# Kernel optimization log

Hardware: AMD Instinct MI355X
Metric: run time of the kernel (lower is better)

Reference implementation:

```python
import jax, jax.numpy as jnp
import numpy as np

N = 100000      # nodes
E = 1600000     # edges (avg degree 16)
G = 500         # graphs in batch
C_IN = 128
H = 128
C_OUT = 200
N_CLASSES = 4


def _lin(k, fi, fo):
    s = 1.0 / np.sqrt(fi)
    return jax.random.uniform(k, (fi, fo), jnp.float32, -s, s)


def setup_inputs() -> dict:
    key = jax.random.key(0)
    ks = jax.random.split(key, 8)
    x = jax.random.normal(ks[0], (N, C_IN), jnp.float32)
    edge_index = jax.random.randint(ks[1], (2, E), 0, N, dtype=jnp.int64)
    edge_attr = jax.random.uniform(ks[2], (E,), jnp.float32)
    batch = jnp.sort(jax.random.randint(ks[3], (N,), 0, G, dtype=jnp.int64))
    W0 = _lin(ks[4], C_IN, H)
    W1 = _lin(ks[5], H, H)
    W2 = _lin(ks[6], H, C_OUT)
    Wp = _lin(ks[7], C_OUT, N_CLASSES)
    return dict(
        x=x, edge_index=edge_index, edge_attr=edge_attr, batch=batch,
        W0=W0, b0=jnp.zeros((H,), jnp.float32),
        W1=W1, b1=jnp.zeros((H,), jnp.float32),
        W2=W2, b2=jnp.zeros((C_OUT,), jnp.float32),
        Wp=Wp, bp=jnp.zeros((N_CLASSES,), jnp.float32),
    )


def reference(x, edge_index, edge_attr, batch, W0, b0, W1, b1, W2, b2, Wp, bp):
    n = x.shape[0]
    loop = jnp.arange(n)
    # GCNConv: add self-loops (weight 1), symmetric normalization D^-1/2 A D^-1/2
    src = jnp.concatenate([edge_index[0], loop])
    dst = jnp.concatenate([edge_index[1], loop])
    w = jnp.concatenate([edge_attr, jnp.ones((n,), x.dtype)])
    deg = jax.ops.segment_sum(w, dst, num_segments=n)
    dis = jnp.where(deg > 0, jax.lax.rsqrt(jnp.maximum(deg, 1e-12)), 0.0)
    norm = dis[src] * w * dis[dst]  # [E+N]

    def conv(h, W, b):
        h = h @ W                               # transform first (PyG GCNConv)
        msg = h[src] * norm[:, None]            # gather + scale
        return jax.ops.segment_sum(msg, dst, num_segments=n) + b

    h = jax.nn.relu(conv(x, W0, b0))
    h = jax.nn.relu(conv(h, W1, b1))
    h = conv(h, W2, b2)                         # last layer: no activation

    # global_mean_pool over graph ids
    gsum = jax.ops.segment_sum(h, batch, num_segments=G)
    cnt = jax.ops.segment_sum(jnp.ones((n,), h.dtype), batch, num_segments=G)
    pooled = gsum / jnp.maximum(cnt, 1.0)[:, None]

    return pooled @ Wp + bp  # [G, 4]
```

## Files before the change

### kernel.cpp

```cpp
#include <hip/hip_runtime.h>
#include <hip/hip_bf16.h>
#include <hip/hip_fp16.h>


#define FEAT 128
#define BSH 8
#define BCAP 8192

typedef union { int2 i2; long long u; struct { int s; float w; } e; } EdgePair;
typedef union { unsigned u; __half2 h2; } H2U;
typedef _Float16 f16x8 __attribute__((ext_vector_type(8)));
typedef float f32x4 __attribute__((ext_vector_type(4)));
typedef float f32x2 __attribute__((ext_vector_type(2)));

__device__ __forceinline__ unsigned pack2h(float a, float b) {
    return (unsigned)__half_as_ushort(__float2half_rn(a)) |
           ((unsigned)__half_as_ushort(__float2half_rn(b)) << 16);
}

__device__ __forceinline__ unsigned char to_fp8(float v) {
    int pk = __builtin_amdgcn_cvt_pk_fp8_f32(v, v, 0, false);
    return (unsigned char)(pk & 0xFF);
}

__global__ __launch_bounds__(256) void bin1_kernel(const int* __restrict__ src,
                                                   const int* __restrict__ dst,
                                                   const float* __restrict__ w,
                                                   int* __restrict__ gcnt,
                                                   int2* __restrict__ bins,
                                                   int E_, int NB) {
    __shared__ int lh[392], lofs[392], lbase[392], lcur[392];
    __shared__ unsigned sU[4096];
    __shared__ float    sW[4096];
    __shared__ unsigned short sB[4096];
    const int CHUNK = 4096;
    int base = blockIdx.x * CHUNK;
    int tid = threadIdx.x;
    for (int t = tid; t < NB; t += 256) { lh[t] = 0; lcur[t] = 0; }
    __syncthreads();
    int ds[16];
#pragma unroll
    for (int j = 0; j < 16; ++j) {
        int e = base + j * 256 + tid;
        ds[j] = (e < E_) ? dst[e] : -1;
        if (ds[j] >= 0) atomicAdd(&lh[ds[j] >> BSH], 1);
    }
    __syncthreads();
    for (int t = tid; t < NB; t += 256) {
        int run = 0;
        for (int i = 0; i < t; ++i) run += lh[i];
        lofs[t] = run;
    }
    __syncthreads();
    for (int t = tid; t < NB; t += 256)
        if (lh[t] > 0) lbase[t] = atomicAdd(&gcnt[t], lh[t]);
    __syncthreads();
#pragma unroll
    for (int j = 0; j < 16; ++j) {
        int e = base + j * 256 + tid;
        if (ds[j] >= 0) {
            int b = ds[j] >> BSH;
            int r = atomicAdd(&lcur[b], 1);
            int s = lofs[b] + r;
            sU[s] = (unsigned)src[e] | ((unsigned)(ds[j] & 255) << 20);
            sW[s] = w[e];
            sB[s] = (unsigned short)b;
        }
    }
    __syncthreads();
    int total = min(CHUNK, E_ - base);
    for (int s = tid; s < total; s += 256) {
        int b = sB[s];
        int g = lbase[b] + (s - lofs[b]);
        if (g < BCAP) {
            int2 val; val.x = (int)sU[s]; val.y = __float_as_int(sW[s]);
            bins[(size_t)b * BCAP + g] = val;
        }
    }
}

__global__ __launch_bounds__(256) void buildcsr_kernel(const int2* __restrict__ bins,
                                                       const int* __restrict__ gcnt,
                                                       int* __restrict__ rp,
                                                       float* __restrict__ dis,
                                                       unsigned* __restrict__ cv, int n) {
    __shared__ int lh[256];
    __shared__ float wsum[256];
    __shared__ int sc[256];
    __shared__ int lcur[256];
    __shared__ int red[256];
    __shared__ unsigned scv[BCAP + 256];
    int b = blockIdx.x;
    int tid = threadIdx.x;
    int node0 = b << BSH;
    int node = node0 + tid;
    bool valid = node < n;
    lh[tid] = 0;
    wsum[tid] = 1.0f;
    int part = 0;
    for (int i = tid; i < b; i += 256)
        part += min(gcnt[i], BCAP) + min(256, n - (i << BSH));
    red[tid] = part;
    __syncthreads();
    for (int off = 128; off > 0; off >>= 1) {
        if (tid < off) red[tid] += red[tid + off];
        __syncthreads();
    }
    int base = red[0];
    int m = min(gcnt[b], BCAP);
    int nvalid = min(256, n - node0);
    if (b == (int)gridDim.x - 1 && tid == 0)
        rp[n] = base + m + nvalid;
    const int2* bp = bins + (size_t)b * BCAP;
    for (int i = tid; i < m; i += 256) {
        int2 raw = bp[i];
        unsigned pk = (unsigned)raw.x;
        int dlo = pk >> 20;
        atomicAdd(&lh[dlo], 1);
        atomicAdd(&wsum[dlo], __int_as_float(raw.y));
    }
    __syncthreads();
    int cnt_t = valid ? (lh[tid] + 1) : 0;
    sc[tid] = cnt_t;
    __syncthreads();
    for (int off = 1; off < 256; off <<= 1) {
        int x = (tid >= off) ? sc[tid - off] : 0;
        __syncthreads();
        sc[tid] += x;
        __syncthreads();
    }
    int excl = sc[tid] - cnt_t;
    if (valid) {
        rp[node] = base + excl;
        dis[node] = rsqrtf(fmaxf(wsum[tid], 1e-12f));
    }
    lcur[tid] = excl;
    __syncthreads();
    for (int i = tid; i < m; i += 256) {
        int2 raw = bp[i];
        unsigned pk = (unsigned)raw.x;
        int dlo = pk >> 20;
        int pos = atomicAdd(&lcur[dlo], 1);
        unsigned hw = (unsigned)__half_as_ushort(__float2half_rn(__int_as_float(raw.y)));
        scv[pos] = (hw << 17) | (pk & 0x1FFFF);
    }
    __syncthreads();
    if (valid) {
        int pos = atomicAdd(&lcur[tid], 1);
        scv[pos] = (0x3C00u << 17) | (unsigned)node;
    }
    __syncthreads();
    int total = m + nvalid;
    for (int s = tid; s < total; s += 256)
        cv[base + s] = scv[s];
}

__global__ __launch_bounds__(256) void prep_kernel(const float* __restrict__ W0,
                                                   const float* __restrict__ W1,
                                                   const float* __restrict__ W2,
                                                   const float* __restrict__ Wp,
                                                   const float* __restrict__ b2,
                                                   const float* __restrict__ bp,
                                                   const int* __restrict__ batch,
                                                   _Float16* __restrict__ Wt0,
                                                   _Float16* __restrict__ Wt1,
                                                   float* __restrict__ Wc,
                                                   float* __restrict__ bc,
                                                   int* __restrict__ gstart,
                                                   int* __restrict__ gcnt,
                                                   int n, int G_, int NB) {
    int blk = blockIdx.x;
    if (blk < 64) {
        int tid = blk * 256 + threadIdx.x;
        int nn = tid >> 7, k = tid & 127;
        Wt0[nn * 128 + k] = (_Float16)W0[k * 128 + nn];
    } else if (blk < 128) {
        int tid = (blk - 64) * 256 + threadIdx.x;
        int nn = tid >> 7, k = tid & 127;
        Wt1[nn * 128 + k] = (_Float16)W1[k * 128 + nn];
    } else if (blk == 128) {
        for (int tid = threadIdx.x; tid < 512; tid += 256) {
            int c = tid >> 2, k = tid & 3;
            float s = 0.f;
            for (int j = 0; j < 200; ++j) s = fmaf(W2[c * 200 + j], Wp[j * 4 + k], s);
            Wc[tid] = s;
        }
        if (threadIdx.x < 4) {
            float s = bp[threadIdx.x];
            for (int j = 0; j < 200; ++j) s = fmaf(b2[j], Wp[j * 4 + threadIdx.x], s);
            bc[threadIdx.x] = s;
        }
        for (int i = threadIdx.x; i < NB; i += 256) gcnt[i] = 0;
    } else {
        int i = (blk - 129) * 256 + threadIdx.x;
        if (i >= n) return;
        int b = batch[i];
        int prev = (i == 0) ? -1 : batch[i - 1];
        for (int g = prev + 1; g <= b; ++g) gstart[g] = i;
        if (i == n - 1) {
            for (int g = b + 1; g <= G_; ++g) gstart[g] = n;
        }
    }
}

__global__ __launch_bounds__(256, 4) void gemm1_mfma(const float* __restrict__ A,
                                                     const _Float16* __restrict__ Wt,
                                                     const float* __restrict__ rowscale,
                                                     unsigned char* __restrict__ C, int M) {
    int wid = threadIdx.x >> 6, lane = threadIdx.x & 63;
    int quad = lane >> 4, l16 = lane & 15;
    int row0 = blockIdx.x * 64 + wid * 16;
    int arow = row0 + l16; if (arow >= M) arow = M - 1;
    const float* abase = A + (size_t)arow * 128 + quad * 8;
    float4 a0[4], a1[4];
#pragma unroll
    for (int kc = 0; kc < 4; ++kc) {
        a0[kc] = *(const float4*)(abase + kc * 32);
        a1[kc] = *(const float4*)(abase + kc * 32 + 4);
    }
    f16x8 af[4];
#pragma unroll
    for (int kc = 0; kc < 4; ++kc)
        af[kc] = (f16x8){ (_Float16)a0[kc].x, (_Float16)a0[kc].y, (_Float16)a0[kc].z, (_Float16)a0[kc].w,
                          (_Float16)a1[kc].x, (_Float16)a1[kc].y, (_Float16)a1[kc].z, (_Float16)a1[kc].w };
    f32x4 acc[8];
#pragma unroll
    for (int t = 0; t < 8; ++t) acc[t] = (f32x4){0.f, 0.f, 0.f, 0.f};
    const _Float16* wbase = Wt + (size_t)l16 * 128 + quad * 8;
#pragma unroll
    for (int t = 0; t < 8; ++t) {
        f16x8 bf[4];
#pragma unroll
        for (int kc = 0; kc < 4; ++kc)
            bf[kc] = *(const f16x8*)(wbase + (size_t)t * 16 * 128 + kc * 32);
#pragma unroll
        for (int kc = 0; kc < 4; ++kc)
            acc[t] = __builtin_amdgcn_mfma_f32_16x16x32_f16(af[kc], bf[kc], acc[t], 0, 0, 0);
    }
    int orow0 = row0 + quad * 4;
#pragma unroll
    for (int r = 0; r < 4; ++r) {
        int orow = orow0 + r;
        if (orow < M) {
            float sc = rowscale[orow];
#pragma unroll
            for (int t = 0; t < 8; ++t)
                C[(size_t)orow * 128 + t * 16 + l16] = to_fp8(acc[t][r] * sc);
        }
    }
}

__global__ __launch_bounds__(256, 4) void gemm2_mfma(const unsigned short* __restrict__ A,
                                                     const _Float16* __restrict__ Wt,
                                                     const float* __restrict__ rowscale,
                                                     unsigned char* __restrict__ C, int M) {
    int wid = threadIdx.x >> 6, lane = threadIdx.x & 63;
    int quad = lane >> 4, l16 = lane & 15;
    int row0 = blockIdx.x * 64 + wid * 16;
    int arow = row0 + l16; if (arow >= M) arow = M - 1;
    const _Float16* abase = (const _Float16*)A + (size_t)arow * 128 + quad * 8;
    f16x8 af[4];
#pragma unroll
    for (int kc = 0; kc < 4; ++kc)
        af[kc] = *(const f16x8*)(abase + kc * 32);
    f32x4 acc[8];
#pragma unroll
    for (int t = 0; t < 8; ++t) acc[t] = (f32x4){0.f, 0.f, 0.f, 0.f};
    const _Float16* wbase = Wt + (size_t)l16 * 128 + quad * 8;
#pragma unroll
    for (int t = 0; t < 8; ++t) {
        f16x8 bf[4];
#pragma unroll
        for (int kc = 0; kc < 4; ++kc)
            bf[kc] = *(const f16x8*)(wbase + (size_t)t * 16 * 128 + kc * 32);
#pragma unroll
        for (int kc = 0; kc < 4; ++kc)
            acc[t] = __builtin_amdgcn_mfma_f32_16x16x32_f16(af[kc], bf[kc], acc[t], 0, 0, 0);
    }
    int orow0 = row0 + quad * 4;
#pragma unroll
    for (int r = 0; r < 4; ++r) {
        int orow = orow0 + r;
        if (orow < M) {
            float sc = rowscale[orow];
#pragma unroll
            for (int t = 0; t < 8; ++t)
                C[(size_t)orow * 128 + t * 16 + l16] = to_fp8(acc[t][r] * sc);
        }
    }
}

__global__ __launch_bounds__(256) void prop_kernel(const int* __restrict__ rp,
                                                   const unsigned* __restrict__ cv,
                                                   const float* __restrict__ dis,
                                                   const unsigned char* __restrict__ t8,
                                                   const float* __restrict__ bias,
                                                   unsigned short* __restrict__ out,
                                                   int off, int lim) {
    int wv = off + ((blockIdx.x * blockDim.x + threadIdx.x) >> 6);
    int lane = threadIdx.x & 63;
    if (wv >= lim) return;
    int half = lane >> 5, l5 = lane & 31;
    int beg = rp[wv], end = rp[wv + 1];
    const unsigned char* tb = t8 + 4 * l5;
    f32x2 aL[4], aH[4];
#pragma unroll
    for (int j = 0; j < 4; ++j) { aL[j] = (f32x2){0.f, 0.f}; aH[j] = (f32x2){0.f, 0.f}; }
    int deg = end - beg;
    int nfull = deg & ~15;
    int p = beg;
    for (; p < beg + nfull; p += 16) {
#pragma unroll
        for (int jj = 0; jj < 8; ++jj) {
            unsigned e = cv[p + 2 * jj + half];
            unsigned v = *(const unsigned*)(tb + ((size_t)(e & 0x1FFFF) << 7));
            float w = __half2float(__ushort_as_half((unsigned short)(e >> 17)));
            f32x2 w2 = {w, w};
            f32x2 lo = __builtin_amdgcn_cvt_pk_f32_fp8((int)v, false);
            f32x2 hi = __builtin_amdgcn_cvt_pk_f32_fp8((int)v, true);
            aL[jj & 3] = lo * w2 + aL[jj & 3];
            aH[jj & 3] = hi * w2 + aH[jj & 3];
        }
    }
    if (p < end) {
        int last = end - 1;
#pragma unroll
        for (int jj = 0; jj < 8; ++jj) {
            int idx = p + 2 * jj + half;
            unsigned e = cv[min(idx, last)];
            unsigned v = *(const unsigned*)(tb + ((size_t)(e & 0x1FFFF) << 7));
            float w = __half2float(__ushort_as_half((unsigned short)(e >> 17)));
            w = (idx < end) ? w : 0.f;
            f32x2 w2 = {w, w};
            f32x2 lo = __builtin_amdgcn_cvt_pk_f32_fp8((int)v, false);
            f32x2 hi = __builtin_amdgcn_cvt_pk_f32_fp8((int)v, true);
            aL[jj & 3] = lo * w2 + aL[jj & 3];
            aH[jj & 3] = hi * w2 + aH[jj & 3];
        }
    }
    f32x2 sL = (aL[0] + aL[1]) + (aL[2] + aL[3]);
    f32x2 sH = (aH[0] + aH[1]) + (aH[2] + aH[3]);
    float s0 = sL[0], s1 = sL[1], s2 = sH[0], s3 = sH[1];
    s0 += __shfl_xor(s0, 32, 64);
    s1 += __shfl_xor(s1, 32, 64);
    s2 += __shfl_xor(s2, 32, 64);
    s3 += __shfl_xor(s3, 32, 64);
    if (half == 0) {
        float dd = dis[wv];
        float4 b = *(const float4*)&bias[4 * l5];
        float r0 = fmaxf(fmaf(dd, s0, b.x), 0.f);
        float r1 = fmaxf(fmaf(dd, s1, b.y), 0.f);
        float r2 = fmaxf(fmaf(dd, s2, b.z), 0.f);
        float r3 = fmaxf(fmaf(dd, s3, b.w), 0.f);
        uint2 pk;
        pk.x = pack2h(r0, r1);
        pk.y = pack2h(r2, r3);
        *(uint2*)&out[(size_t)wv * FEAT + 4 * l5] = pk;
    }
}

__global__ __launch_bounds__(256) void prop_zk_kernel(const int* __restrict__ rp,
                                                      const unsigned* __restrict__ cv,
                                                      const float* __restrict__ dis,
                                                      const unsigned char* __restrict__ t8,
                                                      const float* __restrict__ bias,
                                                      const float* __restrict__ Wc,
                                                      float* __restrict__ z,
                                                      int off, int lim) {
    int wv = off + ((blockIdx.x * blockDim.x + threadIdx.x) >> 6);
    int lane = threadIdx.x & 63;
    if (wv >= lim) return;
    int half = lane >> 5, l5 = lane & 31;
    int beg = rp[wv], end = rp[wv + 1];
    const unsigned char* tb = t8 + 4 * l5;
    f32x2 aL[4], aH[4];
#pragma unroll
    for (int j = 0; j < 4; ++j) { aL[j] = (f32x2){0.f, 0.f}; aH[j] = (f32x2){0.f, 0.f}; }
    int deg = end - beg;
    int nfull = deg & ~15;
    int p = beg;
    for (; p < beg + nfull; p += 16) {
#pragma unroll
        for (int jj = 0; jj < 8; ++jj) {
            unsigned e = cv[p + 2 * jj + half];
            unsigned v = *(const unsigned*)(tb + ((size_t)(e & 0x1FFFF) << 7));
            float w = __half2float(__ushort_as_half((unsigned short)(e >> 17)));
            f32x2 w2 = {w, w};
            f32x2 lo = __builtin_amdgcn_cvt_pk_f32_fp8((int)v, false);
            f32x2 hi = __builtin_amdgcn_cvt_pk_f32_fp8((int)v, true);
            aL[jj & 3] = lo * w2 + aL[jj & 3];
            aH[jj & 3] = hi * w2 + aH[jj & 3];
        }
    }
    if (p < end) {
        int last = end - 1;
#pragma unroll
        for (int jj = 0; jj < 8; ++jj) {
            int idx = p + 2 * jj + half;
            unsigned e = cv[min(idx, last)];
            unsigned v = *(const unsigned*)(tb + ((size_t)(e & 0x1FFFF) << 7));
            float w = __half2float(__ushort_as_half((unsigned short)(e >> 17)));
            w = (idx < end) ? w : 0.f;
            f32x2 w2 = {w, w};
            f32x2 lo = __builtin_amdgcn_cvt_pk_f32_fp8((int)v, false);
            f32x2 hi = __builtin_amdgcn_cvt_pk_f32_fp8((int)v, true);
            aL[jj & 3] = lo * w2 + aL[jj & 3];
            aH[jj & 3] = hi * w2 + aH[jj & 3];
        }
    }
    f32x2 sL = (aL[0] + aL[1]) + (aL[2] + aL[3]);
    f32x2 sH = (aH[0] + aH[1]) + (aH[2] + aH[3]);
    float s0 = sL[0], s1 = sL[1], s2 = sH[0], s3 = sH[1];
    s0 += __shfl_xor(s0, 32, 64);
    s1 += __shfl_xor(s1, 32, 64);
    s2 += __shfl_xor(s2, 32, 64);
    s3 += __shfl_xor(s3, 32, 64);
    float dd = dis[wv];
    float4 b = *(const float4*)&bias[4 * l5];
    float h0 = fmaxf(fmaf(dd, s0, b.x), 0.f);
    float h1 = fmaxf(fmaf(dd, s1, b.y), 0.f);
    float h2 = fmaxf(fmaf(dd, s2, b.z), 0.f);
    float h3 = fmaxf(fmaf(dd, s3, b.w), 0.f);
    float4 w0 = *(const float4*)&Wc[16 * l5];
    float4 w1 = *(const float4*)&Wc[16 * l5 + 4];
    float4 w2 = *(const float4*)&Wc[16 * l5 + 8];
    float4 w3 = *(const float4*)&Wc[16 * l5 + 12];
    float4 par;
    par.x = fmaf(h0, w0.x, fmaf(h1, w1.x, fmaf(h2, w2.x, h3 * w3.x)));
    par.y = fmaf(h0, w0.y, fmaf(h1, w1.y, fmaf(h2, w2.y, h3 * w3.y)));
    par.z = fmaf(h0, w0.z, fmaf(h1, w1.z, fmaf(h2, w2.z, h3 * w3.z)));
    par.w = fmaf(h0, w0.w, fmaf(h1, w1.w, fmaf(h2, w2.w, h3 * w3.w)));
#pragma unroll
    for (int mask = 1; mask < 32; mask <<= 1) {
        par.x += __shfl_xor(par.x, mask, 64);
        par.y += __shfl_xor(par.y, mask, 64);
        par.z += __shfl_xor(par.z, mask, 64);
        par.w += __shfl_xor(par.w, mask, 64);
    }
    if (lane == 0) {
        par.x *= dd; par.y *= dd; par.z *= dd; par.w *= dd;
        *(float4*)&z[(size_t)wv * 4] = par;
    }
}

__global__ __launch_bounds__(256) void prop4_kernel(const int* __restrict__ rp,
                                                    const unsigned* __restrict__ cv,
                                                    const float* __restrict__ dis,
                                                    const float* __restrict__ z,
                                                    float* __restrict__ z2, int n) {
    int i = blockIdx.x * blockDim.x + threadIdx.x;
    if (i >= n) return;
    int beg = rp[i], end = rp[i + 1], last = end - 1;
    float4 a[4];
#pragma unroll
    for (int j = 0; j < 4; ++j) a[j] = (float4){0.f, 0.f, 0.f, 0.f};
    for (int p = beg; p < end; p += 4) {
#pragma unroll
        for (int j = 0; j < 4; ++j) {
            int idx = p + j;
            unsigned e = cv[min(idx, last)];
            float wq = __half2float(__ushort_as_half((unsigned short)(e >> 17)));
            wq = (idx < end) ? wq : 0.f;
            float4 v = *(const float4*)&z[(size_t)(e & 0x1FFFF) * 4];
            a[j].x = fmaf(v.x, wq, a[j].x); a[j].y = fmaf(v.y, wq, a[j].y);
            a[j].z = fmaf(v.z, wq, a[j].z); a[j].w = fmaf(v.w, wq, a[j].w);
        }
    }
    float dd = dis[i];
    float4 r;
    r.x = dd * ((a[0].x + a[1].x) + (a[2].x + a[3].x));
    r.y = dd * ((a[0].y + a[1].y) + (a[2].y + a[3].y));
    r.z = dd * ((a[0].z + a[1].z) + (a[2].z + a[3].z));
    r.w = dd * ((a[0].w + a[1].w) + (a[2].w + a[3].w));
    *(float4*)&z2[(size_t)i * 4] = r;
}

__global__ __launch_bounds__(256) void pool4_kernel(const float* __restrict__ z2,
                                                    const int* __restrict__ gstart,
                                                    const float* __restrict__ bc,
                                                    float* __restrict__ out, int G_) {
    __shared__ float sd[256];
    int g = blockIdx.x;
    int k = threadIdx.x & 3;
    int sub = threadIdx.x >> 2;
    int beg = gstart[g], end = gstart[g + 1];
    float s = 0.f;
    for (int i = beg + sub; i < end; i += 64) s += z2[(size_t)i * 4 + k];
    sd[threadIdx.x] = s;
    __syncthreads();
    for (int off = 32; off > 0; off >>= 1) {
        if (sub < off) sd[threadIdx.x] += sd[threadIdx.x + off * 4];
        __syncthreads();
    }
    if (sub == 0) {
        int c = end - beg;
        out[g * 4 + k] = sd[k] / (float)max(c, 1) + bc[k];
    }
}

extern "C" void kernel_launch(void* const* d_in, const int* in_sizes, int n_in,
                              void* d_out, int out_size, void* d_ws, size_t ws_size,
                              hipStream_t stream) {
    const float* x    = (const float*)d_in[0];
    const int*   ei   = (const int*)d_in[1];
    const float* eatt = (const float*)d_in[2];
    const int*   batch= (const int*)d_in[3];
    const float* W0   = (const float*)d_in[4];
    const float* b0   = (const float*)d_in[5];
    const float* W1   = (const float*)d_in[6];
    const float* b1   = (const float*)d_in[7];
    const float* W2   = (const float*)d_in[8];
    const float* b2   = (const float*)d_in[9];
    const float* Wp   = (const float*)d_in[10];
    const float* bp   = (const float*)d_in[11];
    float* out = (float*)d_out;

    const int Nn = in_sizes[0] / FEAT;
    const int E_ = in_sizes[2];
    const int G_ = out_size / 4;
    const int NNZ = E_ + Nn;
    const int NB = ((Nn - 1) >> BSH) + 1;

    const int* e_src = ei;
    const int* e_dst = ei + E_;

    char* ws = (char*)d_ws;
    size_t off = 0;
    auto alloc = [&](size_t bytes) { void* p = ws + off; off = (off + bytes + 255) & ~(size_t)255; return p; };
    float* dis     = (float*)alloc((size_t)Nn * 4);
    int*   rp      = (int*)  alloc((size_t)(Nn + 1) * 4);
    int*   gcnt    = (int*)  alloc((size_t)NB * 4);
    unsigned* cv   = (unsigned*)alloc((size_t)NNZ * 4);
    unsigned short* bufA = (unsigned short*)alloc((size_t)NB * BCAP * 8);
    unsigned char* bufB8 = (unsigned char*)alloc((size_t)Nn * FEAT);
    int*   gstart  = (int*)  alloc((size_t)(G_ + 1) * 4);
    float* z       = (float*)alloc((size_t)Nn * 4 * 4);
    float* z2      = (float*)alloc((size_t)Nn * 4 * 4);
    float* Wc      = (float*)alloc(512 * 4);
    float* bc      = (float*)alloc(4 * 4);
    _Float16* Wt0  = (_Float16*)alloc(128 * 128 * 2);
    _Float16* Wt1  = (_Float16*)alloc(128 * 128 * 2);
    int2*  bins    = (int2*)bufA;
    (void)ws_size;

    const int T = 256;
    auto cdiv = [](int a, int b) { return (a + b - 1) / b; };
    const int half1 = (Nn + 1) / 2;

    prep_kernel<<<129 + cdiv(Nn, T), T, 0, stream>>>(W0, W1, W2, Wp, b2, bp, batch,
                                                     Wt0, Wt1, Wc, bc, gstart, gcnt,
                                                     Nn, G_, NB);

    bin1_kernel<<<cdiv(E_, 4096), T, 0, stream>>>(e_src, e_dst, eatt, gcnt, bins, E_, NB);
    buildcsr_kernel<<<NB, T, 0, stream>>>(bins, gcnt, rp, dis, cv, Nn);

    gemm1_mfma<<<cdiv(Nn, 64), T, 0, stream>>>(x, Wt0, dis, bufB8, Nn);
    prop_kernel<<<cdiv(half1 * 64, T), T, 0, stream>>>(rp, cv, dis, bufB8, b0, bufA, 0, half1);
    prop_kernel<<<cdiv((Nn - half1) * 64, T), T, 0, stream>>>(rp, cv, dis, bufB8, b0, bufA, half1, Nn);

    gemm2_mfma<<<cdiv(Nn, 64), T, 0, stream>>>(bufA, Wt1, dis, bufB8, Nn);
    prop_zk_kernel<<<cdiv(half1 * 64, T), T, 0, stream>>>(rp, cv, dis, bufB8, b1, Wc, z, 0, half1);
    prop_zk_kernel<<<cdiv((Nn - half1) * 64, T), T, 0, stream>>>(rp, cv, dis, bufB8, b1, Wc, z, half1, Nn);

    prop4_kernel<<<cdiv(Nn, T), T, 0, stream>>>(rp, cv, dis, z, z2, Nn);
    pool4_kernel<<<G_, T, 0, stream>>>(z2, gstart, bc, out, G_);
}
```

Before: 354.9 us.

## Stage GEMM weights in swizzled LDS and shrink edge-binning chunk size

Each GEMM block now copies the 32KB fp16 weight matrix into shared memory with an XOR swizzle and reads the MFMA B fragments from LDS instead of from global/L2. The aim is lower global read traffic and fewer bank conflicts on the B operand. Separately, the binning kernel processes 1024 edges per block instead of 4096, which gives more blocks and more parallelism but also more global atomics on the bin counters. The 32KB LDS per block may reduce GEMM occupancy, and every block pays for the weight copy.

New measurement: 349.9 us. About the same (-1.4%).

```diff
diff --git a/kernel.cpp b/kernel.cpp
--- a/kernel.cpp
+++ b/kernel.cpp
@@ -30,17 +30,17 @@
                                                    int2* __restrict__ bins,
                                                    int E_, int NB) {
     __shared__ int lh[392], lofs[392], lbase[392], lcur[392];
-    __shared__ unsigned sU[4096];
-    __shared__ float    sW[4096];
-    __shared__ unsigned short sB[4096];
-    const int CHUNK = 4096;
+    __shared__ unsigned sU[1024];
+    __shared__ float    sW[1024];
+    __shared__ unsigned short sB[1024];
+    const int CHUNK = 1024;
     int base = blockIdx.x * CHUNK;
     int tid = threadIdx.x;
     for (int t = tid; t < NB; t += 256) { lh[t] = 0; lcur[t] = 0; }
     __syncthreads();
-    int ds[16];
-#pragma unroll
-    for (int j = 0; j < 16; ++j) {
+    int ds[4];
+#pragma unroll
+    for (int j = 0; j < 4; ++j) {
         int e = base + j * 256 + tid;
         ds[j] = (e < E_) ? dst[e] : -1;
         if (ds[j] >= 0) atomicAdd(&lh[ds[j] >> BSH], 1);
@@ -56,7 +56,7 @@
         if (lh[t] > 0) lbase[t] = atomicAdd(&gcnt[t], lh[t]);
     __syncthreads();
 #pragma unroll
-    for (int j = 0; j < 16; ++j) {
+    for (int j = 0; j < 4; ++j) {
         int e = base + j * 256 + tid;
         if (ds[j] >= 0) {
             int b = ds[j] >> BSH;
@@ -207,7 +207,9 @@
                                                      const _Float16* __restrict__ Wt,
                                                      const float* __restrict__ rowscale,
                                                      unsigned char* __restrict__ C, int M) {
-    int wid = threadIdx.x >> 6, lane = threadIdx.x & 63;
+    __shared__ _Float16 sWt[128 * 128];
+    int tid = threadIdx.x;
+    int wid = tid >> 6, lane = tid & 63;
     int quad = lane >> 4, l16 = lane & 15;
     int row0 = blockIdx.x * 64 + wid * 16;
     int arow = row0 + l16; if (arow >= M) arow = M - 1;
@@ -218,6 +220,17 @@
         a0[kc] = *(const float4*)(abase + kc * 32);
         a1[kc] = *(const float4*)(abase + kc * 32 + 4);
     }
+    {
+        const char* s = (const char*)Wt;
+        char* d = (char*)sWt;
+#pragma unroll
+        for (int j = 0; j < 8; ++j) {
+            int o = (tid + j * 256) * 16;
+            int so = o ^ (((o >> 8) & 7) << 4);
+            *(uint4*)(d + so) = *(const uint4*)(s + o);
+        }
+    }
+    __syncthreads();
     f16x8 af[4];
 #pragma unroll
     for (int kc = 0; kc < 4; ++kc)
@@ -226,13 +239,16 @@
     f32x4 acc[8];
 #pragma unroll
     for (int t = 0; t < 8; ++t) acc[t] = (f32x4){0.f, 0.f, 0.f, 0.f};
-    const _Float16* wbase = Wt + (size_t)l16 * 128 + quad * 8;
+    const char* wb = (const char*)sWt;
+    int xorv = (l16 & 7) << 4;
 #pragma unroll
     for (int t = 0; t < 8; ++t) {
         f16x8 bf[4];
 #pragma unroll
-        for (int kc = 0; kc < 4; ++kc)
-            bf[kc] = *(const f16x8*)(wbase + (size_t)t * 16 * 128 + kc * 32);
+        for (int kc = 0; kc < 4; ++kc) {
+            int o = (((t * 16 + l16) * 128 + quad * 8 + kc * 32) * 2) ^ xorv;
+            bf[kc] = *(const f16x8*)(wb + o);
+        }
 #pragma unroll
         for (int kc = 0; kc < 4; ++kc)
             acc[t] = __builtin_amdgcn_mfma_f32_16x16x32_f16(af[kc], bf[kc], acc[t], 0, 0, 0);
@@ -254,7 +270,9 @@
                                                      const _Float16* __restrict__ Wt,
                                                      const float* __restrict__ rowscale,
                                                      unsigned char* __restrict__ C, int M) {
-    int wid = threadIdx.x >> 6, lane = threadIdx.x & 63;
+    __shared__ _Float16 sWt[128 * 128];
+    int tid = threadIdx.x;
+    int wid = tid >> 6, lane = tid & 63;
     int quad = lane >> 4, l16 = lane & 15;
     int row0 = blockIdx.x * 64 + wid * 16;
     int arow = row0 + l16; if (arow >= M) arow = M - 1;
@@ -263,16 +281,30 @@
 #pragma unroll
     for (int kc = 0; kc < 4; ++kc)
         af[kc] = *(const f16x8*)(abase + kc * 32);
+    {
+        const char* s = (const char*)Wt;
+        char* d = (char*)sWt;
+#pragma unroll
+        for (int j = 0; j < 8; ++j) {
+            int o = (tid + j * 256) * 16;
+            int so = o ^ (((o >> 8) & 7) << 4);
+            *(uint4*)(d + so) = *(const uint4*)(s + o);
+        }
+    }
+    __syncthreads();
     f32x4 acc[8];
 #pragma unroll
     for (int t = 0; t < 8; ++t) acc[t] = (f32x4){0.f, 0.f, 0.f, 0.f};
-    const _Float16* wbase = Wt + (size_t)l16 * 128 + quad * 8;
+    const char* wb = (const char*)sWt;
+    int xorv = (l16 & 7) << 4;
 #pragma unroll
     for (int t = 0; t < 8; ++t) {
         f16x8 bf[4];
 #pragma unroll
-        for (int kc = 0; kc < 4; ++kc)
-            bf[kc] = *(const f16x8*)(wbase + (size_t)t * 16 * 128 + kc * 32);
+        for (int kc = 0; kc < 4; ++kc) {
+            int o = (((t * 16 + l16) * 128 + quad * 8 + kc * 32) * 2) ^ xorv;
+            bf[kc] = *(const f16x8*)(wb + o);
+        }
 #pragma unroll
         for (int kc = 0; kc < 4; ++kc)
             acc[t] = __builtin_amdgcn_mfma_f32_16x16x32_f16(af[kc], bf[kc], acc[t], 0, 0, 0);
@@ -551,7 +583,7 @@
                                                      Wt0, Wt1, Wc, bc, gstart, gcnt,
                                                      Nn, G_, NB);
 
-    bin1_kernel<<<cdiv(E_, 4096), T, 0, stream>>>(e_src, e_dst, eatt, gcnt, bins, E_, NB);
+    bin1_kernel<<<cdiv(E_, 1024), T, 0, stream>>>(e_src, e_dst, eatt, gcnt, bins, E_, NB);
     buildcsr_kernel<<<NB, T, 0, stream>>>(bins, gcnt, rp, dis, cv, Nn);
 
     gemm1_mfma<<<cdiv(Nn, 64), T, 0, stream>>>(x, Wt0, dis, bufB8, Nn);
```
